# Optimization experiments

Hardware: AMD Instinct MI355X
Metric: run time of the kernel (lower is better)

The kernel has to match this reference:

```python
import jax, jax.numpy as jnp
import numpy as np

B, S, D, V, N_BLOCKS = 4096, 128, 9, 5, 4


def _pos_encoding(seq_len, dim):
    pos = jnp.arange(seq_len, dtype=jnp.float32)[:, None]
    d = jnp.arange(dim)[None, :]
    angle = pos / jnp.power(10000.0, (2.0 * (d // 2)) / dim).astype(jnp.float32)
    return jnp.where(d % 2 == 0, jnp.sin(angle), jnp.cos(angle))  # [S, D]


def setup_inputs() -> dict:
    key = jax.random.key(0)
    ks = jax.random.split(key, 10)
    sc = 1.0 / np.sqrt(D)
    return {
        "tokens": jax.random.randint(ks[0], (B, S), 0, V),
        "emb": jax.random.normal(ks[1], (V, D), jnp.float32),
        "Wq": jax.random.normal(ks[2], (N_BLOCKS, D, D), jnp.float32) * sc,
        "bq": jax.random.normal(ks[3], (N_BLOCKS, D), jnp.float32) * sc,
        "Wk": jax.random.normal(ks[4], (N_BLOCKS, D, D), jnp.float32) * sc,
        "bk": jax.random.normal(ks[5], (N_BLOCKS, D), jnp.float32) * sc,
        "Wv": jax.random.normal(ks[6], (N_BLOCKS, D, D), jnp.float32) * sc,
        "bv": jax.random.normal(ks[7], (N_BLOCKS, D), jnp.float32) * sc,
        "Wout": jax.random.normal(ks[8], (V, D), jnp.float32) * sc,
        "bout": jax.random.normal(ks[9], (V,), jnp.float32) * sc,
    }


def reference(tokens, emb, Wq, bq, Wk, bk, Wv, bv, Wout, bout):
    seq_len = tokens.shape[1]
    x = emb[tokens] + _pos_encoding(S, D)[:seq_len]  # [B, S, D]
    scale = 1.0 / jnp.sqrt(jnp.asarray(D, x.dtype))
    for i in range(N_BLOCKS):
        # torch Linear: y = x @ W.T + b
        Q = jnp.einsum('bsd,ed->bse', x, Wq[i]) + bq[i]
        K = jnp.einsum('bsd,ed->bse', x, Wk[i]) + bk[i]
        Vv = jnp.einsum('bsd,ed->bse', x, Wv[i]) + bv[i]
        scores = jnp.einsum('bqd,bkd->bqk', Q, K) * scale  # [B, S, S]
        probs = jax.nn.softmax(scores, axis=-1)
        x = jnp.einsum('bqk,bkd->bqd', probs, Vv)
    logits = jnp.einsum('bsd,vd->bsv', x, Wout) + bout  # [B, S, V]
    return jax.nn.log_softmax(logits, axis=-1)
```

## Files before the change

kernel.cpp:

```cpp
#include <hip/hip_runtime.h>
#include <math.h>

constexpr int Bn = 4096;
constexpr int Sn = 128;
constexpr int Dn = 9;
constexpr int Vn = 5;
constexpr int NBn = 4;

typedef float f4 __attribute__((ext_vector_type(4)));
typedef _Float16 h8 __attribute__((ext_vector_type(8)));
typedef __fp16   h2 __attribute__((ext_vector_type(2)));
typedef unsigned u4v __attribute__((ext_vector_type(4)));
typedef short s4v __attribute__((ext_vector_type(4)));

constexpr int KF_OFF = 0;
constexpr int QF_OFF = 10240;
constexpr int VF_OFF = 20480;
constexpr int XB_OFF = 24832;
constexpr int SMEM_BYTES = 30976;

static __device__ __forceinline__ void split_hl(const float* v, _Float16* H, _Float16* L) {
    #pragma unroll
    for (int i = 0; i < 9; ++i) {
        _Float16 h = (_Float16)v[i];
        H[i] = h;
        L[i] = (_Float16)(v[i] - (float)h);
    }
}

static __device__ __forceinline__ unsigned pk(_Float16 a, _Float16 b) {
    h2 t; t.x = (__fp16)a; t.y = (__fp16)b;
    return __builtin_bit_cast(unsigned, t);
}

static __device__ __forceinline__ void store_3term_row(short* rowp,
        const _Float16* X, const _Float16* Y, const _Float16* Z) {
    const _Float16 z0 = (_Float16)0.0f;
    u4v w0 = (u4v){ pk(X[0],X[1]), pk(X[2],X[3]), pk(X[4],X[5]), pk(X[6],X[7]) };
    u4v w1 = (u4v){ pk(X[8],Y[0]), pk(Y[1],Y[2]), pk(Y[3],Y[4]), pk(Y[5],Y[6]) };
    u4v w2 = (u4v){ pk(Y[7],Y[8]), pk(Z[0],Z[1]), pk(Z[2],Z[3]), pk(Z[4],Z[5]) };
    u4v w3 = (u4v){ pk(Z[6],Z[7]), pk(Z[8],z0),   0u,            0u            };
    u4v* qp = (u4v*)rowp;
    qp[0] = w0; qp[1] = w1; qp[2] = w2; qp[3] = w3;
}

static __device__ __forceinline__ h8 read_quad(const short* base, int row, int quad) {
    return *(const h8*)(base + row * 40 + quad * 8);
}

__global__ __launch_bounds__(256, 4) void bert_kernel(
    const int*   __restrict__ tokens,
    const float* __restrict__ emb,
    const float* __restrict__ Wq, const float* __restrict__ bq,
    const float* __restrict__ Wk, const float* __restrict__ bk,
    const float* __restrict__ Wv, const float* __restrict__ bv,
    const float* __restrict__ Wout, const float* __restrict__ bout,
    float*       __restrict__ out)
{
    __shared__ __align__(16) char smem[SMEM_BYTES];
    short* KF = (short*)(smem + KF_OFF);
    short* QF = (short*)(smem + QF_OFF);
    short* VF = (short*)(smem + VF_OFF);
    float* XB = (float*)(smem + XB_OFF);

    const int b   = blockIdx.x;
    const int tid = threadIdx.x;
    const int t   = tid & 63;
    const int w   = tid >> 6;
    const int col = t & 15;
    const int g   = t >> 4;
    const bool lowhalf = tid < 128;
    const int r = lowhalf ? tid : tid - 128;
    const float qscale = (1.0f / 3.0f) * 1.44269504f;

    if (lowhalf) {
        const float inv_freq[Dn] = {
            1.0f, 1.0f,
            0.1291549665f, 0.1291549665f,
            0.0166810054f, 0.0166810054f,
            0.0021544347f, 0.0021544347f,
            0.0002782559f
        };
        const int tok = tokens[b * Sn + r];
        float xr[9];
        #pragma unroll
        for (int d = 0; d < Dn; ++d) {
            const float a = (float)r * inv_freq[d];
            const float p = (d & 1) ? cosf(a) : sinf(a);
            xr[d] = emb[tok * Dn + d] + p;
        }
        f4* xp = (f4*)&XB[r * 12];
        xp[0] = (f4){xr[0], xr[1], xr[2], xr[3]};
        xp[1] = (f4){xr[4], xr[5], xr[6], xr[7]};
        xp[2] = (f4){xr[8], 0.0f, 0.0f, 0.0f};
    }
    __syncthreads();

    #pragma unroll 1
    for (int it = 0; it < NBn; ++it) {
        {
            const f4* xp = (const f4*)&XB[r * 12];
            f4 a0 = xp[0], a1 = xp[1], a2 = xp[2];
            float x[9] = {a0.x, a0.y, a0.z, a0.w, a1.x, a1.y, a1.z, a1.w, a2.x};
            const float* wv  = Wv + it * 81;
            const float* bvi = bv + it * 9;
            if (lowhalf) {
                const float* wk  = Wk + it * 81;
                const float* bki = bk + it * 9;
                float kv[9];
                #pragma unroll
                for (int e = 0; e < Dn; ++e) {
                    float ak = bki[e];
                    #pragma unroll
                    for (int d = 0; d < Dn; ++d) ak = fmaf(x[d], wk[e * 9 + d], ak);
                    kv[e] = ak;
                }
                _Float16 H[9], L[9];
                split_hl(kv, H, L);
                store_3term_row(KF + r * 40, H, H, L);
                #pragma unroll
                for (int e = 0; e < 4; ++e) {
                    float av = bvi[e];
                    #pragma unroll
                    for (int d = 0; d < Dn; ++d) av = fmaf(x[d], wv[e * 9 + d], av);
                    VF[e * 136 + r] = __builtin_bit_cast(short, (_Float16)av);
                }
            } else {
                const float* wq  = Wq + it * 81;
                const float* bqi = bq + it * 9;
                float qv[9];
                #pragma unroll
                for (int e = 0; e < Dn; ++e) {
                    float aq = bqi[e];
                    #pragma unroll
                    for (int d = 0; d < Dn; ++d) aq = fmaf(x[d], wq[e * 9 + d], aq);
                    qv[e] = aq * qscale;
                }
                _Float16 H[9], L[9];
                split_hl(qv, H, L);
                store_3term_row(QF + r * 40, H, L, H);
                #pragma unroll
                for (int e = 4; e < Dn; ++e) {
                    float av = bvi[e];
                    #pragma unroll
                    for (int d = 0; d < Dn; ++d) av = fmaf(x[d], wv[e * 9 + d], av);
                    VF[e * 136 + r] = __builtin_bit_cast(short, (_Float16)av);
                }
            }
        }
        __syncthreads();

        h8 kfr[8];
        #pragma unroll
        for (int kt = 0; kt < 8; ++kt)
            kfr[kt] = read_quad(KF, kt * 16 + col, g);

        h8 vf[4];
        #pragma unroll
        for (int s = 0; s < 4; ++s) {
            const short* p0 = VF + col * 136 + 32 * s + 4 * g;
            s4v va = *(const s4v*)p0;
            s4v vb = *(const s4v*)(p0 + 16);
            vf[s] = __builtin_bit_cast(h8,
                __builtin_shufflevector(va, vb, 0, 1, 2, 3, 4, 5, 6, 7));
        }

        #pragma unroll
        for (int ti = 0; ti < 2; ++ti) {
            const int qt = 2 * w + ti;
            const int q  = qt * 16 + col;
            h8 bq3 = read_quad(QF, q, g);

            f4 acc[8];
            #pragma unroll
            for (int kt = 0; kt < 8; ++kt)
                acc[kt] = __builtin_amdgcn_mfma_f32_16x16x32_f16(kfr[kt], bq3, (f4)(0.0f), 0, 0, 0);

            f4 m0 = __builtin_elementwise_max(acc[0], acc[1]);
            f4 m1 = __builtin_elementwise_max(acc[2], acc[3]);
            f4 m2 = __builtin_elementwise_max(acc[4], acc[5]);
            f4 m3 = __builtin_elementwise_max(acc[6], acc[7]);
            f4 m4 = __builtin_elementwise_max(__builtin_elementwise_max(m0, m1),
                                              __builtin_elementwise_max(m2, m3));
            float mx = fmaxf(fmaxf(m4.x, m4.y), fmaxf(m4.z, m4.w));
            mx = fmaxf(mx, __shfl_xor(mx, 16));
            mx = fmaxf(mx, __shfl_xor(mx, 32));

            f4 sv = (f4)(0.0f);
            #pragma unroll
            for (int kt = 0; kt < 8; ++kt) {
                f4 e;
                #pragma unroll
                for (int rr = 0; rr < 4; ++rr)
                    e[rr] = __builtin_amdgcn_exp2f(acc[kt][rr] - mx);
                acc[kt] = e;
                sv += e;
            }
            float sm = (sv.x + sv.y) + (sv.z + sv.w);
            sm += __shfl_xor(sm, 16);
            sm += __shfl_xor(sm, 32);

            f4 oac = (f4)(0.0f);
            #pragma unroll
            for (int s = 0; s < 4; ++s) {
                u4v up = (u4v){
                    __builtin_bit_cast(unsigned, __builtin_amdgcn_cvt_pkrtz(acc[2*s][0],   acc[2*s][1])),
                    __builtin_bit_cast(unsigned, __builtin_amdgcn_cvt_pkrtz(acc[2*s][2],   acc[2*s][3])),
                    __builtin_bit_cast(unsigned, __builtin_amdgcn_cvt_pkrtz(acc[2*s+1][0], acc[2*s+1][1])),
                    __builtin_bit_cast(unsigned, __builtin_amdgcn_cvt_pkrtz(acc[2*s+1][2], acc[2*s+1][3])) };
                oac = __builtin_amdgcn_mfma_f32_16x16x32_f16(vf[s], __builtin_bit_cast(h8, up), oac, 0, 0, 0);
            }
            const float rl = 1.0f / sm;
            oac *= rl;
            if (g < 3)
                *(f4*)&XB[q * 12 + g * 4] = oac;
        }
        __syncthreads();
    }

    if (lowhalf) {
        const f4* xp = (const f4*)&XB[r * 12];
        f4 a0 = xp[0], a1 = xp[1], a2 = xp[2];
        float xr[9] = {a0.x, a0.y, a0.z, a0.w, a1.x, a1.y, a1.z, a1.w, a2.x};
        float lg[Vn];
        #pragma unroll
        for (int v = 0; v < Vn; ++v) {
            float a = bout[v];
            #pragma unroll
            for (int d = 0; d < Dn; ++d) a = fmaf(xr[d], Wout[v * Dn + d], a);
            lg[v] = a;
        }
        float mm = lg[0];
        #pragma unroll
        for (int v = 1; v < Vn; ++v) mm = fmaxf(mm, lg[v]);
        float sum = 0.0f;
        #pragma unroll
        for (int v = 0; v < Vn; ++v)
            sum += __builtin_amdgcn_exp2f((lg[v] - mm) * 1.44269504f);
        const float lse = __builtin_amdgcn_logf(sum) * 0.69314718f + mm;
        float* op = out + ((size_t)b * Sn + r) * Vn;
        #pragma unroll
        for (int v = 0; v < Vn; ++v) op[v] = lg[v] - lse;
    }
}

extern "C" void kernel_launch(void* const* d_in, const int* in_sizes, int n_in,
                              void* d_out, int out_size, void* d_ws, size_t ws_size,
                              hipStream_t stream) {
    const int*   tokens = (const int*)  d_in[0];
    const float* emb    = (const float*)d_in[1];
    const float* Wq     = (const float*)d_in[2];
    const float* bq_    = (const float*)d_in[3];
    const float* Wk     = (const float*)d_in[4];
    const float* bk_    = (const float*)d_in[5];
    const float* Wv     = (const float*)d_in[6];
    const float* bv_    = (const float*)d_in[7];
    const float* Wout   = (const float*)d_in[8];
    const float* bout_  = (const float*)d_in[9];
    float* out = (float*)d_out;

    bert_kernel<<<dim3(Bn), dim3(256), 0, stream>>>(
        tokens, emb, Wq, bq_, Wk, bk_, Wv, bv_, Wout, bout_, out);
}
```

Baseline: 150.9 us.

## Fold Wk^T Wq into a precomputed bilinear form and derive softmax sum from MFMA

A small prep kernel computes M = Wk^T·Wq (scaled) and the bias term Wk^T·bq per block, plus a positional-encoding table, into workspace. The main kernel then uses raw x as the key side and x·M plus bias as the query side, packing the bias term into the spare K slot of the f16 MFMA. Terms that are constant per query row, including those involving bk, are dropped because softmax cancels them. A ones row is added to V so the PV MFMA also yields the softmax denominator, which removes the shuffle reductions. It rebalances the V projection across the two thread halves, adds an extra launch, and uses an approximate reciprocal.

```diff
diff --git a/kernel.cpp b/kernel.cpp
--- a/kernel.cpp
+++ b/kernel.cpp
@@ -12,6 +12,8 @@
 typedef __fp16   h2 __attribute__((ext_vector_type(2)));
 typedef unsigned u4v __attribute__((ext_vector_type(4)));
 typedef short s4v __attribute__((ext_vector_type(4)));
+
+constexpr int WS_PE = 384;
 
 constexpr int KF_OFF = 0;
 constexpr int QF_OFF = 10240;
@@ -33,28 +35,60 @@
     return __builtin_bit_cast(unsigned, t);
 }
 
-static __device__ __forceinline__ void store_3term_row(short* rowp,
-        const _Float16* X, const _Float16* Y, const _Float16* Z) {
+static __device__ __forceinline__ void store_row32(short* rowp,
+        const _Float16* X, const _Float16* Y, const _Float16* Z,
+        _Float16 T0, _Float16 T1) {
     const _Float16 z0 = (_Float16)0.0f;
     u4v w0 = (u4v){ pk(X[0],X[1]), pk(X[2],X[3]), pk(X[4],X[5]), pk(X[6],X[7]) };
     u4v w1 = (u4v){ pk(X[8],Y[0]), pk(Y[1],Y[2]), pk(Y[3],Y[4]), pk(Y[5],Y[6]) };
     u4v w2 = (u4v){ pk(Y[7],Y[8]), pk(Z[0],Z[1]), pk(Z[2],Z[3]), pk(Z[4],Z[5]) };
-    u4v w3 = (u4v){ pk(Z[6],Z[7]), pk(Z[8],z0),   0u,            0u            };
+    u4v w3 = (u4v){ pk(Z[6],Z[7]), pk(Z[8],T0),   pk(T1,z0),     0u            };
     u4v* qp = (u4v*)rowp;
     qp[0] = w0; qp[1] = w1; qp[2] = w2; qp[3] = w3;
 }
 
 static __device__ __forceinline__ h8 read_quad(const short* base, int row, int quad) {
     return *(const h8*)(base + row * 40 + quad * 8);
+}
+
+__global__ void prep_kernel(const float* __restrict__ Wq, const float* __restrict__ bq,
+                            const float* __restrict__ Wk, float* __restrict__ ws)
+{
+    const float qs = (1.0f / 3.0f) * 1.44269504f;
+    const int idx = blockIdx.x * 256 + threadIdx.x;
+    if (idx < 360) {
+        const int it = idx / 90, j = idx % 90;
+        const float* wq = Wq + it * 81;
+        const float* wk = Wk + it * 81;
+        float acc = 0.0f;
+        if (j < 81) {
+            const int e = j / 9, d = j % 9;
+            #pragma unroll
+            for (int f = 0; f < 9; ++f) acc = fmaf(wk[f * 9 + e], wq[f * 9 + d], acc);
+        } else {
+            const int d = j - 81;
+            const float* bqp = bq + it * 9;
+            #pragma unroll
+            for (int f = 0; f < 9; ++f) acc = fmaf(wk[f * 9 + d], bqp[f], acc);
+        }
+        ws[it * 96 + j] = acc * qs;
+    } else if (idx < 360 + Sn * Dn) {
+        const int j = idx - 360;
+        const int r = j / 9, d = j % 9;
+        const float inv_freq[Dn] = {
+            1.0f, 1.0f, 0.1291549665f, 0.1291549665f, 0.0166810054f,
+            0.0166810054f, 0.0021544347f, 0.0021544347f, 0.0002782559f };
+        const float a = (float)r * inv_freq[d];
+        ws[WS_PE + j] = (d & 1) ? cosf(a) : sinf(a);
+    }
 }
 
 __global__ __launch_bounds__(256, 4) void bert_kernel(
     const int*   __restrict__ tokens,
     const float* __restrict__ emb,
-    const float* __restrict__ Wq, const float* __restrict__ bq,
-    const float* __restrict__ Wk, const float* __restrict__ bk,
     const float* __restrict__ Wv, const float* __restrict__ bv,
     const float* __restrict__ Wout, const float* __restrict__ bout,
+    const float* __restrict__ wsp,
     float*       __restrict__ out)
 {
     __shared__ __align__(16) char smem[SMEM_BYTES];
@@ -71,28 +105,21 @@
     const int g   = t >> 4;
     const bool lowhalf = tid < 128;
     const int r = lowhalf ? tid : tid - 128;
-    const float qscale = (1.0f / 3.0f) * 1.44269504f;
+    const float* MP = wsp;
+    const float* PE = wsp + WS_PE;
 
     if (lowhalf) {
-        const float inv_freq[Dn] = {
-            1.0f, 1.0f,
-            0.1291549665f, 0.1291549665f,
-            0.0166810054f, 0.0166810054f,
-            0.0021544347f, 0.0021544347f,
-            0.0002782559f
-        };
         const int tok = tokens[b * Sn + r];
         float xr[9];
         #pragma unroll
-        for (int d = 0; d < Dn; ++d) {
-            const float a = (float)r * inv_freq[d];
-            const float p = (d & 1) ? cosf(a) : sinf(a);
-            xr[d] = emb[tok * Dn + d] + p;
-        }
+        for (int d = 0; d < Dn; ++d)
+            xr[d] = emb[tok * Dn + d] + PE[r * 9 + d];
         f4* xp = (f4*)&XB[r * 12];
         xp[0] = (f4){xr[0], xr[1], xr[2], xr[3]};
         xp[1] = (f4){xr[4], xr[5], xr[6], xr[7]};
         xp[2] = (f4){xr[8], 0.0f, 0.0f, 0.0f};
+    } else {
+        VF[9 * 136 + r] = (short)0x3C00;
     }
     __syncthreads();
 
@@ -104,48 +131,40 @@
             float x[9] = {a0.x, a0.y, a0.z, a0.w, a1.x, a1.y, a1.z, a1.w, a2.x};
             const float* wv  = Wv + it * 81;
             const float* bvi = bv + it * 9;
+            const float* mp  = MP + it * 96;
             if (lowhalf) {
-                const float* wk  = Wk + it * 81;
-                const float* bki = bk + it * 9;
-                float kv[9];
-                #pragma unroll
-                for (int e = 0; e < Dn; ++e) {
-                    float ak = bki[e];
-                    #pragma unroll
-                    for (int d = 0; d < Dn; ++d) ak = fmaf(x[d], wk[e * 9 + d], ak);
-                    kv[e] = ak;
-                }
+                float tb = 0.0f;
+                #pragma unroll
+                for (int d = 0; d < Dn; ++d) tb = fmaf(x[d], mp[81 + d], tb);
                 _Float16 H[9], L[9];
-                split_hl(kv, H, L);
-                store_3term_row(KF + r * 40, H, H, L);
-                #pragma unroll
-                for (int e = 0; e < 4; ++e) {
+                split_hl(x, H, L);
+                _Float16 th = (_Float16)tb;
+                _Float16 tl = (_Float16)(tb - (float)th);
+                store_row32(KF + r * 40, H, H, L, th, tl);
+                #pragma unroll
+                for (int e = 0; e < 8; ++e) {
                     float av = bvi[e];
                     #pragma unroll
                     for (int d = 0; d < Dn; ++d) av = fmaf(x[d], wv[e * 9 + d], av);
                     VF[e * 136 + r] = __builtin_bit_cast(short, (_Float16)av);
                 }
             } else {
-                const float* wq  = Wq + it * 81;
-                const float* bqi = bq + it * 9;
-                float qv[9];
+                float y[9];
                 #pragma unroll
                 for (int e = 0; e < Dn; ++e) {
-                    float aq = bqi[e];
+                    float a = 0.0f;
                     #pragma unroll
-                    for (int d = 0; d < Dn; ++d) aq = fmaf(x[d], wq[e * 9 + d], aq);
-                    qv[e] = aq * qscale;
+                    for (int d = 0; d < Dn; ++d) a = fmaf(x[d], mp[e * 9 + d], a);
+                    y[e] = a;
                 }
                 _Float16 H[9], L[9];
-                split_hl(qv, H, L);
-                store_3term_row(QF + r * 40, H, L, H);
-                #pragma unroll
-                for (int e = 4; e < Dn; ++e) {
-                    float av = bvi[e];
-                    #pragma unroll
-                    for (int d = 0; d < Dn; ++d) av = fmaf(x[d], wv[e * 9 + d], av);
-                    VF[e * 136 + r] = __builtin_bit_cast(short, (_Float16)av);
-                }
+                split_hl(y, H, L);
+                store_row32(QF + r * 40, H, L, H,
+                            (_Float16)1.0f, (_Float16)1.0f);
+                float av = bvi[8];
+                #pragma unroll
+                for (int d = 0; d < Dn; ++d) av = fmaf(x[d], wv[8 * 9 + d], av);
+                VF[8 * 136 + r] = __builtin_bit_cast(short, (_Float16)av);
             }
         }
         __syncthreads();
@@ -186,19 +205,11 @@
             mx = fmaxf(mx, __shfl_xor(mx, 16));
             mx = fmaxf(mx, __shfl_xor(mx, 32));
 
-            f4 sv = (f4)(0.0f);
-            #pragma unroll
-            for (int kt = 0; kt < 8; ++kt) {
-                f4 e;
+            #pragma unroll
+            for (int kt = 0; kt < 8; ++kt)
                 #pragma unroll
                 for (int rr = 0; rr < 4; ++rr)
-                    e[rr] = __builtin_amdgcn_exp2f(acc[kt][rr] - mx);
-                acc[kt] = e;
-                sv += e;
-            }
-            float sm = (sv.x + sv.y) + (sv.z + sv.w);
-            sm += __shfl_xor(sm, 16);
-            sm += __shfl_xor(sm, 32);
+                    acc[kt][rr] = __builtin_amdgcn_exp2f(acc[kt][rr] - mx);
 
             f4 oac = (f4)(0.0f);
             #pragma unroll
@@ -210,7 +221,8 @@
                     __builtin_bit_cast(unsigned, __builtin_amdgcn_cvt_pkrtz(acc[2*s+1][2], acc[2*s+1][3])) };
                 oac = __builtin_amdgcn_mfma_f32_16x16x32_f16(vf[s], __builtin_bit_cast(h8, up), oac, 0, 0, 0);
             }
-            const float rl = 1.0f / sm;
+            const float sm = __shfl(oac[1], 32 + col);
+            const float rl = __builtin_amdgcn_rcpf(sm);
             oac *= rl;
             if (g < 3)
                 *(f4*)&XB[q * 12 + g * 4] = oac;
@@ -252,13 +264,14 @@
     const float* Wq     = (const float*)d_in[2];
     const float* bq_    = (const float*)d_in[3];
     const float* Wk     = (const float*)d_in[4];
-    const float* bk_    = (const float*)d_in[5];
     const float* Wv     = (const float*)d_in[6];
     const float* bv_    = (const float*)d_in[7];
     const float* Wout   = (const float*)d_in[8];
     const float* bout_  = (const float*)d_in[9];
     float* out = (float*)d_out;
-
+    float* ws  = (float*)d_ws;
+
+    prep_kernel<<<dim3(6), dim3(256), 0, stream>>>(Wq, bq_, Wk, ws);
     bert_kernel<<<dim3(Bn), dim3(256), 0, stream>>>(
-        tokens, emb, Wq, bq_, Wk, bk_, Wv, bv_, Wout, bout_, out);
-}
+        tokens, emb, Wv, bv_, Wout, bout_, ws, out);
+}
```

Result: faster. 140.8 us (-6.7%).
